# Performance work log

Hardware: AMD Instinct MI355X
Metric: run time of the kernel (lower is better)

Reference implementation:

```python
import jax, jax.numpy as jnp
import numpy as np

N_NODES = 50000
N_EDGES = 800000
D_IN, H, D_OUT = 128, 128, 64


def setup_inputs() -> dict:
    key = jax.random.key(0)
    ks = jax.random.split(key, 8)
    x = jax.random.normal(ks[0], (N_NODES, D_IN), dtype=jnp.float32)
    edge_index = jax.random.randint(ks[1], (2, N_EDGES), 0, N_NODES, dtype=jnp.int64)
    s = 0.05
    return {
        "x": x,
        "edge_index": edge_index,
        # PyG Linear weights are [out, in]; y = x @ W.T + b
        "W_rel1": jax.random.normal(ks[2], (H, D_IN), dtype=jnp.float32) * s,
        "W_root1": jax.random.normal(ks[3], (H, D_IN), dtype=jnp.float32) * s,
        "b1": jax.random.normal(ks[4], (H,), dtype=jnp.float32) * s,
        "W_rel2": jax.random.normal(ks[5], (D_OUT, H), dtype=jnp.float32) * s,
        "W_root2": jax.random.normal(ks[6], (D_OUT, H), dtype=jnp.float32) * s,
        "b2": jax.random.normal(ks[7], (D_OUT,), dtype=jnp.float32) * s,
    }


def graph_conv(x, src, dst, W_rel, W_root, b):
    # sum-aggregate raw neighbor features, then apply linear (equivalent to
    # transforming each message first, but cheaper: one gather + one GEMM).
    agg = jax.ops.segment_sum(x[src], dst, num_segments=N_NODES)  # [N, D]
    return jnp.einsum('nd,hd->nh', agg, W_rel) \
         + jnp.einsum('nd,hd->nh', x, W_root) + b


def reference(x, edge_index, W_rel1, W_root1, b1, W_rel2, W_root2, b2):
    src, dst = edge_index[0], edge_index[1]  # messages flow src -> dst
    t = jax.nn.relu(graph_conv(x, src, dst, W_rel1, W_root1, b1))
    t = graph_conv(t, src, dst, W_rel2, W_root2, b2)
    return t
```

## Files before the change

### kernel.cpp

```cpp
#include <hip/hip_runtime.h>

#define NNODES 50000
#define DIM 128
#define SCAN_CHUNK 4096
#define NSCAN 13
#define PREP_BLOCKS 3200

typedef __attribute__((ext_vector_type(8))) __bf16 bf16x8;
typedef __attribute__((ext_vector_type(4))) float f32x4;

__device__ inline unsigned short f2b(float f) {
    unsigned int u = __float_as_uint(f);
    u += 0x7fffu + ((u >> 16) & 1u);
    return (unsigned short)(u >> 16);
}
__device__ inline float blo(unsigned int u) { return __uint_as_float(u << 16); }
__device__ inline float bhi(unsigned int u) { return __uint_as_float(u & 0xffff0000u); }
__device__ inline unsigned int pack2(float a, float b) {
    return (unsigned int)f2b(a) | ((unsigned int)f2b(b) << 16);
}

__global__ __launch_bounds__(256) void k_prep(
    const float* __restrict__ x, unsigned short* __restrict__ xb, int n4,
    const float* __restrict__ Wa1, const float* __restrict__ Wb1,
    const float* __restrict__ Wa2, const float* __restrict__ Wb2,
    unsigned short* __restrict__ wa1, unsigned short* __restrict__ wb1,
    unsigned short* __restrict__ wa2, unsigned short* __restrict__ wb2,
    const int* __restrict__ dst, int* __restrict__ counts,
    int* __restrict__ rank, int n_edges)
{
    const int gid = blockIdx.x * 256 + threadIdx.x;

    const int i1 = blockIdx.x * 512 + threadIdx.x;
    const int i2 = i1 + 256;
    const bool ok1 = i1 < n4, ok2 = i2 < n4;
    float4 v1, v2;
    if (ok1) v1 = reinterpret_cast<const float4*>(x)[i1];
    if (ok2) v2 = reinterpret_cast<const float4*>(x)[i2];

    if (gid < n_edges) rank[gid] = atomicAdd(&counts[dst[gid]], 1);

    if (gid < 16384) { wa1[gid] = f2b(Wa1[gid]); wb1[gid] = f2b(Wb1[gid]); }
    if (gid < 8192)  { wa2[gid] = f2b(Wa2[gid]); wb2[gid] = f2b(Wb2[gid]); }

    if (ok1) {
        uint2 o;
        o.x = pack2(v1.x, v1.y);
        o.y = pack2(v1.z, v1.w);
        reinterpret_cast<uint2*>(xb)[i1] = o;
    }
    if (ok2) {
        uint2 o;
        o.x = pack2(v2.x, v2.y);
        o.y = pack2(v2.z, v2.w);
        reinterpret_cast<uint2*>(xb)[i2] = o;
    }
}

__global__ __launch_bounds__(1024) void k_scan_local(
    const int* __restrict__ counts, int* __restrict__ rowptr,
    int* __restrict__ bsum, int n)
{
    __shared__ int wsum[16];
    const int lane = threadIdx.x & 63;
    const int wid = threadIdx.x >> 6;
    int i = blockIdx.x * SCAN_CHUNK + threadIdx.x * 4;
    int4 v = make_int4(0, 0, 0, 0);
    if (i + 3 < n) {
        v = *reinterpret_cast<const int4*>(counts + i);
    } else {
        if (i + 0 < n) v.x = counts[i + 0];
        if (i + 1 < n) v.y = counts[i + 1];
        if (i + 2 < n) v.z = counts[i + 2];
    }
    int tot = v.x + v.y + v.z + v.w;
    int s = tot;
#pragma unroll
    for (int off = 1; off < 64; off <<= 1) {
        int t = __shfl_up(s, off);
        if (lane >= off) s += t;
    }
    if (lane == 63) wsum[wid] = s;
    __syncthreads();
    if (wid == 0 && lane < 16) {
        int ws = wsum[lane];
#pragma unroll
        for (int off = 1; off < 16; off <<= 1) {
            int t = __shfl_up(ws, off);
            if (lane >= off) ws += t;
        }
        wsum[lane] = ws;
    }
    __syncthreads();
    int prefix = ((wid > 0) ? wsum[wid - 1] : 0) + (s - tot);
    int4 o;
    o.x = prefix;
    o.y = prefix + v.x;
    o.z = o.y + v.y;
    o.w = o.z + v.z;
    if (i + 3 <= n) {
        *reinterpret_cast<int4*>(rowptr + i) = o;
    } else {
        if (i + 0 <= n) rowptr[i + 0] = o.x;
        if (i + 1 <= n) rowptr[i + 1] = o.y;
        if (i + 2 <= n) rowptr[i + 2] = o.z;
    }
    if (threadIdx.x == 1023) bsum[blockIdx.x] = wsum[15];
}

__device__ inline void build_prefix_lds(const int* __restrict__ bsum, int* pre) {
    if (threadIdx.x < 16) {
        int off = 0;
#pragma unroll 1
        for (int j = 0; j < NSCAN && j < (int)threadIdx.x; ++j) off += bsum[j];
        pre[threadIdx.x] = off;
    }
    __syncthreads();
}

__global__ __launch_bounds__(256) void k_place(
    const int* __restrict__ src, const int* __restrict__ dst,
    const int* __restrict__ rank, const int* __restrict__ rowptr,
    const int* __restrict__ bsum, int* __restrict__ srcs_sorted, int n_edges)
{
    __shared__ int pre[16];
    build_prefix_lds(bsum, pre);
    int e = (blockIdx.x * 256 + threadIdx.x) * 8;
    if (e + 7 < n_edges) {
        int4 s4a = *reinterpret_cast<const int4*>(src + e);
        int4 s4b = *reinterpret_cast<const int4*>(src + e + 4);
        int4 d4a = *reinterpret_cast<const int4*>(dst + e);
        int4 d4b = *reinterpret_cast<const int4*>(dst + e + 4);
        int4 r4a = *reinterpret_cast<const int4*>(rank + e);
        int4 r4b = *reinterpret_cast<const int4*>(rank + e + 4);
        srcs_sorted[rowptr[d4a.x] + pre[d4a.x >> 12] + r4a.x] = s4a.x;
        srcs_sorted[rowptr[d4a.y] + pre[d4a.y >> 12] + r4a.y] = s4a.y;
        srcs_sorted[rowptr[d4a.z] + pre[d4a.z >> 12] + r4a.z] = s4a.z;
        srcs_sorted[rowptr[d4a.w] + pre[d4a.w >> 12] + r4a.w] = s4a.w;
        srcs_sorted[rowptr[d4b.x] + pre[d4b.x >> 12] + r4b.x] = s4b.x;
        srcs_sorted[rowptr[d4b.y] + pre[d4b.y >> 12] + r4b.y] = s4b.y;
        srcs_sorted[rowptr[d4b.z] + pre[d4b.z >> 12] + r4b.z] = s4b.z;
        srcs_sorted[rowptr[d4b.w] + pre[d4b.w >> 12] + r4b.w] = s4b.w;
    } else {
        for (; e < n_edges; ++e) {
            int d = dst[e];
            srcs_sorted[rowptr[d] + pre[d >> 12] + rank[e]] = src[e];
        }
    }
}

__global__ __launch_bounds__(256) void k_gather_sum(
    const unsigned short* __restrict__ xb, const int* __restrict__ rowptr,
    const int* __restrict__ bsum, const int* __restrict__ srcs,
    unsigned short* __restrict__ aggb)
{
    __shared__ int pre[16];
    build_prefix_lds(bsum, pre);
    int node = blockIdx.x * 16 + (threadIdx.x >> 4);
    if (node >= NNODES) return;
    int seg = threadIdx.x & 15;
    int beg = rowptr[node] + pre[node >> 12];
    int end = rowptr[node + 1] + pre[(node + 1) >> 12];
    float acc[8];
#pragma unroll
    for (int i = 0; i < 8; ++i) acc[i] = 0.f;
    int e = beg;
#pragma unroll 1
    for (; e + 7 < end; e += 8) {
        uint4 v[8];
#pragma unroll
        for (int u = 0; u < 8; ++u) {
            int s = srcs[e + u];
            v[u] = *reinterpret_cast<const uint4*>(xb + (size_t)s * DIM + seg * 8);
        }
#pragma unroll
        for (int u = 0; u < 8; ++u) {
            acc[0] += blo(v[u].x); acc[1] += bhi(v[u].x);
            acc[2] += blo(v[u].y); acc[3] += bhi(v[u].y);
            acc[4] += blo(v[u].z); acc[5] += bhi(v[u].z);
            acc[6] += blo(v[u].w); acc[7] += bhi(v[u].w);
        }
    }
#pragma unroll 1
    for (; e + 1 < end; e += 2) {
        int s0 = srcs[e], s1 = srcs[e + 1];
        uint4 v0 = *reinterpret_cast<const uint4*>(xb + (size_t)s0 * DIM + seg * 8);
        uint4 v1 = *reinterpret_cast<const uint4*>(xb + (size_t)s1 * DIM + seg * 8);
        acc[0] += blo(v0.x) + blo(v1.x); acc[1] += bhi(v0.x) + bhi(v1.x);
        acc[2] += blo(v0.y) + blo(v1.y); acc[3] += bhi(v0.y) + bhi(v1.y);
        acc[4] += blo(v0.z) + blo(v1.z); acc[5] += bhi(v0.z) + bhi(v1.z);
        acc[6] += blo(v0.w) + blo(v1.w); acc[7] += bhi(v0.w) + bhi(v1.w);
    }
    if (e < end) {
        int s0 = srcs[e];
        uint4 v = *reinterpret_cast<const uint4*>(xb + (size_t)s0 * DIM + seg * 8);
        acc[0] += blo(v.x); acc[1] += bhi(v.x);
        acc[2] += blo(v.y); acc[3] += bhi(v.y);
        acc[4] += blo(v.z); acc[5] += bhi(v.z);
        acc[6] += blo(v.w); acc[7] += bhi(v.w);
    }
    uint4 o;
    o.x = pack2(acc[0], acc[1]);
    o.y = pack2(acc[2], acc[3]);
    o.z = pack2(acc[4], acc[5]);
    o.w = pack2(acc[6], acc[7]);
    *reinterpret_cast<uint4*>(aggb + (size_t)node * DIM + seg * 8) = o;
}

template <int BN, bool RELU, bool OUTBF16>
__global__ __launch_bounds__(256) void k_gemm_direct(
    const unsigned short* __restrict__ Ab,
    const unsigned short* __restrict__ Bb,
    const unsigned short* __restrict__ Wa,
    const unsigned short* __restrict__ Wb,
    const float* __restrict__ bias, void* __restrict__ Cout, int n_nodes)
{
    constexpr int NT = BN / 16;
    const int tid = threadIdx.x;
    const int wave = tid >> 6;
    const int lane = tid & 63;
    const int quad = lane >> 4;
    const int l16 = lane & 15;
    const int n0 = blockIdx.x * 64;
    const int arow = n0 + wave * 16 + l16;
    const bool ok = arow < n_nodes;

    f32x4 acc[NT];
#pragma unroll
    for (int nt = 0; nt < NT; ++nt) {
        f32x4 z = {0.f, 0.f, 0.f, 0.f};
        acc[nt] = z;
    }

#pragma unroll 1
    for (int ks = 0; ks < 8; ++ks) {
        const unsigned short* __restrict__ Asrc = (ks < 4) ? Ab : Bb;
        const unsigned short* __restrict__ Wsrc = (ks < 4) ? Wa : Wb;
        const int ko = (ks & 3) * 32;
        bf16x8 a = {};
        if (ok)
            a = *reinterpret_cast<const bf16x8*>(
                Asrc + (size_t)arow * DIM + ko + quad * 8);
#pragma unroll
        for (int nt = 0; nt < NT; ++nt) {
            bf16x8 b = *reinterpret_cast<const bf16x8*>(
                Wsrc + (size_t)(nt * 16 + l16) * DIM + ko + quad * 8);
            acc[nt] = __builtin_amdgcn_mfma_f32_16x16x32_bf16(a, b, acc[nt], 0, 0, 0);
        }
    }

#pragma unroll
    for (int nt = 0; nt < NT; ++nt) {
        int col = nt * 16 + l16;
        float bv = bias[col];
#pragma unroll
        for (int reg = 0; reg < 4; ++reg) {
            int row = n0 + wave * 16 + quad * 4 + reg;
            if (row >= n_nodes) continue;
            float v = acc[nt][reg] + bv;
            if (RELU) v = fmaxf(v, 0.f);
            if (OUTBF16)
                ((unsigned short*)Cout)[(size_t)row * BN + col] = f2b(v);
            else
                ((float*)Cout)[(size_t)row * BN + col] = v;
        }
    }
}

extern "C" void kernel_launch(void* const* d_in, const int* in_sizes, int n_in,
                              void* d_out, int out_size, void* d_ws, size_t ws_size,
                              hipStream_t stream) {
    const float* x       = (const float*)d_in[0];
    const int*   ei      = (const int*)d_in[1];
    const float* W_rel1  = (const float*)d_in[2];
    const float* W_root1 = (const float*)d_in[3];
    const float* b1      = (const float*)d_in[4];
    const float* W_rel2  = (const float*)d_in[5];
    const float* W_root2 = (const float*)d_in[6];
    const float* b2      = (const float*)d_in[7];

    const int n_edges = in_sizes[1] / 2;
    const int* src = ei;
    const int* dst = ei + n_edges;

    const size_t NELEM = (size_t)NNODES * DIM;
    unsigned short* xb   = (unsigned short*)d_ws;
    unsigned short* aggb = xb + NELEM;
    unsigned short* tb   = aggb + NELEM;
    unsigned short* wa1  = tb + NELEM;
    unsigned short* wb1  = wa1 + 16384;
    unsigned short* wa2  = wb1 + 16384;
    unsigned short* wb2  = wa2 + 8192;
    int* counts = (int*)(wb2 + 8192);
    int* rowptr = counts + NNODES;
    int* bsum   = rowptr + (NNODES + 4);
    int* rank   = bsum + 20;
    int* srcs   = rank + n_edges;

    float* out = (float*)d_out;

    const int n4 = NNODES * DIM / 4;
    const int pblocks = (n_edges + 2047) / 2048;
    const int gblocks = (NNODES + 15) / 16;
    const int gemm_blocks = (NNODES + 63) / 64;
    const int sblocks = NSCAN;

    hipMemsetAsync(counts, 0, NNODES * sizeof(int), stream);
    k_prep<<<PREP_BLOCKS, 256, 0, stream>>>(
        x, xb, n4, W_rel1, W_root1, W_rel2, W_root2,
        wa1, wb1, wa2, wb2, dst, counts, rank, n_edges);

    k_scan_local<<<sblocks, 1024, 0, stream>>>(counts, rowptr, bsum, NNODES);
    k_place<<<pblocks, 256, 0, stream>>>(src, dst, rank, rowptr, bsum, srcs, n_edges);

    k_gather_sum<<<gblocks, 256, 0, stream>>>(xb, rowptr, bsum, srcs, aggb);
    k_gemm_direct<128, true, true><<<gemm_blocks, 256, 0, stream>>>(
        aggb, xb, wa1, wb1, b1, tb, NNODES);

    k_gather_sum<<<gblocks, 256, 0, stream>>>(tb, rowptr, bsum, srcs, aggb);
    k_gemm_direct<64, false, false><<<gemm_blocks, 256, 0, stream>>>(
        aggb, tb, wa2, wb2, b2, out, NNODES);
}
```

Before: 260.3 us.

## Assign one wavefront per node in gather-sum with cross-slot shuffle reduction

The gather-sum kernel now gives each node a full 64-lane wave instead of 16 lanes. Four 16-lane slots each handle a different neighbor edge at once, and the partial sums are combined with xor shuffles before one slot writes the result. This is meant to balance the skewed degree distribution and raise memory-level parallelism per node, since the average degree is about 16. In exchange, per-thread unrolling drops from 8 outstanding loads to 2, there is added shuffle-reduction overhead, and four times as many blocks are launched.

```diff
diff --git a/kernel.cpp b/kernel.cpp
--- a/kernel.cpp
+++ b/kernel.cpp
@@ -156,34 +156,24 @@
 {
     __shared__ int pre[16];
     build_prefix_lds(bsum, pre);
-    int node = blockIdx.x * 16 + (threadIdx.x >> 4);
+    const int wave = threadIdx.x >> 6;
+    const int lane = threadIdx.x & 63;
+    const int slot = lane >> 4;
+    const int seg = lane & 15;
+    int node = blockIdx.x * 4 + wave;
     if (node >= NNODES) return;
-    int seg = threadIdx.x & 15;
     int beg = rowptr[node] + pre[node >> 12];
     int end = rowptr[node + 1] + pre[(node + 1) >> 12];
+
     float acc[8];
 #pragma unroll
     for (int i = 0; i < 8; ++i) acc[i] = 0.f;
-    int e = beg;
+
+    int base = beg;
 #pragma unroll 1
-    for (; e + 7 < end; e += 8) {
-        uint4 v[8];
-#pragma unroll
-        for (int u = 0; u < 8; ++u) {
-            int s = srcs[e + u];
-            v[u] = *reinterpret_cast<const uint4*>(xb + (size_t)s * DIM + seg * 8);
-        }
-#pragma unroll
-        for (int u = 0; u < 8; ++u) {
-            acc[0] += blo(v[u].x); acc[1] += bhi(v[u].x);
-            acc[2] += blo(v[u].y); acc[3] += bhi(v[u].y);
-            acc[4] += blo(v[u].z); acc[5] += bhi(v[u].z);
-            acc[6] += blo(v[u].w); acc[7] += bhi(v[u].w);
-        }
-    }
-#pragma unroll 1
-    for (; e + 1 < end; e += 2) {
-        int s0 = srcs[e], s1 = srcs[e + 1];
+    for (; base + 8 <= end; base += 8) {
+        int s0 = srcs[base + slot];
+        int s1 = srcs[base + 4 + slot];
         uint4 v0 = *reinterpret_cast<const uint4*>(xb + (size_t)s0 * DIM + seg * 8);
         uint4 v1 = *reinterpret_cast<const uint4*>(xb + (size_t)s1 * DIM + seg * 8);
         acc[0] += blo(v0.x) + blo(v1.x); acc[1] += bhi(v0.x) + bhi(v1.x);
@@ -191,20 +181,31 @@
         acc[4] += blo(v0.z) + blo(v1.z); acc[5] += bhi(v0.z) + bhi(v1.z);
         acc[6] += blo(v0.w) + blo(v1.w); acc[7] += bhi(v0.w) + bhi(v1.w);
     }
-    if (e < end) {
-        int s0 = srcs[e];
-        uint4 v = *reinterpret_cast<const uint4*>(xb + (size_t)s0 * DIM + seg * 8);
-        acc[0] += blo(v.x); acc[1] += bhi(v.x);
-        acc[2] += blo(v.y); acc[3] += bhi(v.y);
-        acc[4] += blo(v.z); acc[5] += bhi(v.z);
-        acc[6] += blo(v.w); acc[7] += bhi(v.w);
-    }
-    uint4 o;
-    o.x = pack2(acc[0], acc[1]);
-    o.y = pack2(acc[2], acc[3]);
-    o.z = pack2(acc[4], acc[5]);
-    o.w = pack2(acc[6], acc[7]);
-    *reinterpret_cast<uint4*>(aggb + (size_t)node * DIM + seg * 8) = o;
+#pragma unroll
+    for (int t = 0; t < 2; ++t) {
+        int idx = base + t * 4 + slot;
+        if (idx < end) {
+            int s0 = srcs[idx];
+            uint4 v = *reinterpret_cast<const uint4*>(xb + (size_t)s0 * DIM + seg * 8);
+            acc[0] += blo(v.x); acc[1] += bhi(v.x);
+            acc[2] += blo(v.y); acc[3] += bhi(v.y);
+            acc[4] += blo(v.z); acc[5] += bhi(v.z);
+            acc[6] += blo(v.w); acc[7] += bhi(v.w);
+        }
+    }
+#pragma unroll
+    for (int i = 0; i < 8; ++i) {
+        acc[i] += __shfl_xor(acc[i], 16);
+        acc[i] += __shfl_xor(acc[i], 32);
+    }
+    if (slot == 0) {
+        uint4 o;
+        o.x = pack2(acc[0], acc[1]);
+        o.y = pack2(acc[2], acc[3]);
+        o.z = pack2(acc[4], acc[5]);
+        o.w = pack2(acc[6], acc[7]);
+        *reinterpret_cast<uint4*>(aggb + (size_t)node * DIM + seg * 8) = o;
+    }
 }
 
 template <int BN, bool RELU, bool OUTBF16>
@@ -301,7 +302,7 @@
 
     const int n4 = NNODES * DIM / 4;
     const int pblocks = (n_edges + 2047) / 2048;
-    const int gblocks = (NNODES + 15) / 16;
+    const int gblocks = (NNODES + 3) / 4;
     const int gemm_blocks = (NNODES + 63) / 64;
     const int sblocks = NSCAN;
 
```

Measured after the change: 264.5 us. Within noise of the previous version (+1.6%).
